# Kernel optimization log

Measured on AMD Instinct MI355X. Metric: run time of the kernel, lower is better.

## Reference

```python
import jax, jax.numpy as jnp
import numpy as np

B, N, H = 64, 512, 1024
NH = 8            # attention heads
HD = H // NH      # head dim
STEPS = 24


def setup_inputs() -> dict:
    key = jax.random.key(0)
    ks = jax.random.split(key, 12)
    s = 0.05  # weight scale to keep gates/softmax in a sane range
    return {
        "encoder_outputs": jax.random.normal(ks[0], (B, N, H), dtype=jnp.float32),
        "hidden": jax.random.normal(ks[1], (B, H), dtype=jnp.float32) * s,
        "cell": jax.random.normal(ks[2], (B, H), dtype=jnp.float32) * s,
        "end_node_embed": jax.random.normal(ks[3], (B, H), dtype=jnp.float32),
        "initial_input": jax.random.normal(ks[4], (B, 3 * H), dtype=jnp.float32),
        "max_steps": STEPS,
        # LSTMCell params (torch layout: [4H, in], gate order i,f,g,o)
        "W_ih": jax.random.normal(ks[5], (4 * H, 3 * H), dtype=jnp.float32) * s,
        "b_ih": jnp.zeros((4 * H,), jnp.float32),
        "W_hh": jax.random.normal(ks[6], (4 * H, H), dtype=jnp.float32) * s,
        "b_hh": jnp.zeros((4 * H,), jnp.float32),
        # MultiheadAttention params (torch in_proj [3H,H] = [Wq;Wk;Wv])
        "attn_in_w": jax.random.normal(ks[7], (3 * H, H), dtype=jnp.float32) * s,
        "attn_in_b": jnp.zeros((3 * H,), jnp.float32),
        "attn_out_w": jax.random.normal(ks[8], (H, H), dtype=jnp.float32) * s,
        "attn_out_b": jnp.zeros((H,), jnp.float32),
        # query_transform Linear
        "qt_w": jax.random.normal(ks[9], (H, H), dtype=jnp.float32) * s,
        "qt_b": jnp.zeros((H,), jnp.float32),
    }


def reference(encoder_outputs, hidden, cell, end_node_embed, initial_input,
              max_steps, W_ih, b_ih, W_hh, b_hh,
              attn_in_w, attn_in_b, attn_out_w, attn_out_b, qt_w, qt_b):
    b, n, h = encoder_outputs.shape
    nh, hd = NH, H // NH
    Wq, Wk, Wv = jnp.split(attn_in_w, 3, axis=0)
    bq, bk, bv = jnp.split(attn_in_b, 3)
    S = max_steps
    dt = encoder_outputs.dtype
    buf0 = jnp.zeros((b, S, h), dt)  # preallocated KV cache of decoder hiddens
    neg = jnp.asarray(-1e30, dt)
    scale = 1.0 / jnp.sqrt(jnp.asarray(hd, dt))
    pos = jnp.arange(S)

    def step(carry, t):
        hn, cn, x, buf = carry
        # --- LSTMCell (torch gate order i,f,g,o) ---
        gates = x @ W_ih.T + b_ih + hn @ W_hh.T + b_hh
        i, f, g, o = jnp.split(gates, 4, axis=-1)
        cn = jax.nn.sigmoid(f) * cn + jax.nn.sigmoid(i) * jnp.tanh(g)
        hn = jax.nn.sigmoid(o) * jnp.tanh(cn)
        buf = buf.at[:, t, :].set(hn)
        # --- causal self-attention: q = current hidden, kv = all hiddens <= t ---
        q = (hn @ Wq.T + bq).reshape(b, nh, hd)
        k = (buf @ Wk.T + bk).reshape(b, S, nh, hd)
        v = (buf @ Wv.T + bv).reshape(b, S, nh, hd)
        scores = jnp.einsum('bhd,bshd->bhs', q, k) * scale
        scores = jnp.where((pos > t)[None, None, :], neg, scores)
        attn = jax.nn.softmax(scores, axis=-1)
        ctx = jnp.einsum('bhs,bshd->bhd', attn, v).reshape(b, h)
        attn_out = ctx @ attn_out_w.T + attn_out_b
        # --- pointer scoring ---
        query = (0.5 * (hn + attn_out)) @ qt_w.T + qt_b
        logits = jnp.einsum('bh,bnh->bn', query, encoder_outputs)  # [B,N]
        _, idx = jax.lax.top_k(logits, 3)
        idx = jnp.sort(idx, axis=1)
        top3 = jnp.take_along_axis(encoder_outputs, idx[:, :, None], axis=1)  # [B,3,H]
        x = top3.reshape(b, 3 * h)
        return (hn, cn, x, buf), (logits, idx)

    _, (logits, idx) = jax.lax.scan(
        step, (hidden, cell, initial_input, buf0), jnp.arange(S))
    return logits, idx  # [max_steps,B,N], [max_steps,B,3]
```

## Files before the change

kernel.cpp:

```cpp
#include <hip/hip_runtime.h>
#include <math.h>

#define B_  64
#define N_  512
#define H_  1024
#define NH_ 8
#define HD_ 128
#define S_  24

__global__ __launch_bounds__(256) void wc_pre(
    const float* __restrict__ Wqt, const float* __restrict__ Wout,
    const float* __restrict__ bout, const float* __restrict__ bqt,
    float* __restrict__ W2, float* __restrict__ bc)
{
  __shared__ float As[16][68];
  __shared__ float Bs[16][68];
  const int tid = threadIdx.x;
  const int k0 = (blockIdx.x & 15) * 64;
  const int n0 = (blockIdx.x >> 4) * 64;
  const int tn = tid & 15, tm = tid >> 4;

#pragma unroll
  for (int i = 0; i < 4; ++i) {
    int n = n0 + tm * 4 + i;
    float4 w = *(const float4*)(Wqt + (size_t)n * 1024 + k0 + tn * 4);
    *(float4*)(W2 + (size_t)n * 2048 + k0 + tn * 4) =
        make_float4(0.5f * w.x, 0.5f * w.y, 0.5f * w.z, 0.5f * w.w);
  }

  float acc[4][4];
#pragma unroll
  for (int i = 0; i < 4; ++i)
#pragma unroll
    for (int j = 0; j < 4; ++j) acc[i][j] = 0.f;

  for (int m0 = 0; m0 < 1024; m0 += 16) {
    {
      int nn = tid >> 2, mm = (tid & 3) * 4;
      float4 a = *(const float4*)(Wqt + (size_t)(n0 + nn) * 1024 + m0 + mm);
      As[mm + 0][nn] = a.x; As[mm + 1][nn] = a.y;
      As[mm + 2][nn] = a.z; As[mm + 3][nn] = a.w;
      int mr = tid >> 4, kc = (tid & 15) * 4;
      float4 b = *(const float4*)(Wout + (size_t)(m0 + mr) * 1024 + k0 + kc);
      *(float4*)(&Bs[mr][kc]) = b;
    }
    __syncthreads();
#pragma unroll
    for (int m = 0; m < 16; ++m) {
      float av[4], bv[4];
      *(float4*)av = *(const float4*)(&As[m][tm * 4]);
      *(float4*)bv = *(const float4*)(&Bs[m][tn * 4]);
#pragma unroll
      for (int i = 0; i < 4; ++i)
#pragma unroll
        for (int j = 0; j < 4; ++j)
          acc[i][j] = fmaf(av[i], bv[j], acc[i][j]);
    }
    __syncthreads();
  }
#pragma unroll
  for (int i = 0; i < 4; ++i) {
    int n = n0 + tm * 4 + i;
    *(float4*)(W2 + (size_t)n * 2048 + 1024 + k0 + tn * 4) =
        make_float4(0.5f * acc[i][0], 0.5f * acc[i][1],
                    0.5f * acc[i][2], 0.5f * acc[i][3]);
  }

  {
    int w = tid >> 6, lane = tid & 63;
    int n = blockIdx.x * 4 + w;
    const float* row = Wqt + (size_t)n * 1024;
    float s = 0.f;
#pragma unroll
    for (int c = 0; c < 4; ++c) {
      float4 a = *(const float4*)(row + lane * 16 + c * 4);
      float4 b = *(const float4*)(bout + lane * 16 + c * 4);
      s = fmaf(a.x, b.x, fmaf(a.y, b.y, fmaf(a.z, b.z, fmaf(a.w, b.w, s))));
    }
#pragma unroll
    for (int off = 32; off > 0; off >>= 1) s += __shfl_down(s, off, 64);
    if (lane == 0) bc[n] = 0.5f * s + bqt[n];
  }
}

__device__ __forceinline__ float sigm(float x) { return 1.f / (1.f + expf(-x)); }

__device__ __forceinline__ void ins3(float v, int i,
    float& v0, int& i0, float& v1, int& i1, float& v2, int& i2)
{
  if (v > v0 || (v == v0 && i < i0)) {
    v2 = v1; i2 = i1; v1 = v0; i1 = i0; v0 = v; i0 = i;
  } else if (v > v1 || (v == v1 && i < i1)) {
    v2 = v1; i2 = i1; v1 = v; i1 = i;
  } else if (v > v2 || (v == v2 && i < i2)) {
    v2 = v; i2 = i;
  }
}

__global__ __launch_bounds__(512, 2) void gemm5(
    const float* __restrict__ A0, int ldA0, const float* __restrict__ W0, int ldW0,
    int K0,
    const float* __restrict__ A1, int ldA1, const float* __restrict__ W1, int ldW1,
    const float* __restrict__ enc, const int* __restrict__ idxi, int gather,
    float* __restrict__ P, int N, int KS)
{
  __shared__ float As[16 * 68];
  __shared__ float Bs[16 * 132];
  const int tid = threadIdx.x;
  const int nb = blockIdx.x, sp = blockIdx.y;
  const int ks = sp * KS;

  const float* A; const float* W; int ldA, ldW, koff; int seg0;
  if (ks < K0) { A = A0; W = W0; ldA = ldA0; ldW = ldW0; koff = ks; seg0 = 1; }
  else { A = A1; W = W1; ldA = ldA1; ldW = ldW1; koff = ks - K0; seg0 = 0; }

  const int tn = tid & 31, tm = tid >> 5;
  const int lr = tid >> 2, lc = (tid & 3) * 4;

  float acc[4][4];
#pragma unroll
  for (int i = 0; i < 4; ++i)
#pragma unroll
    for (int j = 0; j < 4; ++j) acc[i][j] = 0.f;

  const float* Wrow = W + (size_t)(nb * 128 + lr) * ldW + koff + lc;
  const float* Arow = nullptr;
  if (tid < 256) {
    if (seg0 && gather) {
      int ei = idxi[lr * 3 + (koff >> 10)];
      Arow = enc + ((size_t)lr * 512 + ei) * 1024 + (koff & 1023) + lc;
    } else {
      Arow = A + (size_t)lr * ldA + koff + lc;
    }
  }

  for (int k0 = 0; k0 < KS; k0 += 16) {
    float4 b4 = *(const float4*)(Wrow + k0);
    if (tid < 256) {
      float4 a4 = *(const float4*)(Arow + k0);
      As[(lc + 0) * 68 + lr] = a4.x; As[(lc + 1) * 68 + lr] = a4.y;
      As[(lc + 2) * 68 + lr] = a4.z; As[(lc + 3) * 68 + lr] = a4.w;
    }
    Bs[(lc + 0) * 132 + lr] = b4.x; Bs[(lc + 1) * 132 + lr] = b4.y;
    Bs[(lc + 2) * 132 + lr] = b4.z; Bs[(lc + 3) * 132 + lr] = b4.w;
    __syncthreads();
#pragma unroll
    for (int k = 0; k < 16; ++k) {
      float av[4], bv[4];
      *(float4*)av = *(const float4*)(As + k * 68 + tm * 4);
      *(float4*)bv = *(const float4*)(Bs + k * 132 + tn * 4);
#pragma unroll
      for (int i = 0; i < 4; ++i)
#pragma unroll
        for (int j = 0; j < 4; ++j)
          acc[i][j] = fmaf(av[i], bv[j], acc[i][j]);
    }
    __syncthreads();
  }
  float* Pb = P + (size_t)sp * 64 * N + nb * 128;
#pragma unroll
  for (int i = 0; i < 4; ++i)
    *(float4*)(Pb + (size_t)(tm * 4 + i) * N + tn * 4) =
        make_float4(acc[i][0], acc[i][1], acc[i][2], acc[i][3]);
}

__global__ __launch_bounds__(256) void lstm_red(
    const float* __restrict__ P, const float* __restrict__ b_ih,
    const float* __restrict__ b_hh, const float* __restrict__ c_in,
    float* __restrict__ h_out, float* __restrict__ c_out)
{
  int idx = blockIdx.x * 256 + threadIdx.x;
  int b = idx >> 8, j4 = (idx & 255) * 4;
  float g[4][4];
#pragma unroll
  for (int c = 0; c < 4; ++c) {
    int n = c * 1024 + j4;
    float4 s = *(const float4*)(b_ih + n);
    float4 s2 = *(const float4*)(b_hh + n);
    s.x += s2.x; s.y += s2.y; s.z += s2.z; s.w += s2.w;
#pragma unroll
    for (int sp = 0; sp < 8; ++sp) {
      float4 v = *(const float4*)(P + ((size_t)sp * 64 + b) * 4096 + n);
      s.x += v.x; s.y += v.y; s.z += v.z; s.w += v.w;
    }
    g[c][0] = s.x; g[c][1] = s.y; g[c][2] = s.z; g[c][3] = s.w;
  }
  float4 cp = *(const float4*)(c_in + b * 1024 + j4);
  float cv[4] = {cp.x, cp.y, cp.z, cp.w};
  float4 ho, co;
  float* hp = &ho.x; float* cpn = &co.x;
#pragma unroll
  for (int e = 0; e < 4; ++e) {
    float c = sigm(g[1][e]) * cv[e] + sigm(g[0][e]) * tanhf(g[2][e]);
    cpn[e] = c;
    hp[e] = sigm(g[3][e]) * tanhf(c);
  }
  *(float4*)(c_out + b * 1024 + j4) = co;
  *(float4*)(h_out + b * 1024 + j4) = ho;
}

__global__ __launch_bounds__(128) void attn_fused(
    const float* __restrict__ P, const float* __restrict__ bqkv,
    float* __restrict__ Kc, float* __restrict__ Vc,
    float* __restrict__ ctx, int t)
{
  const float scale = 0.08838834764831845f;
  int bh = blockIdx.x;
  int b = bh >> 3, h = bh & 7;
  int d = threadIdx.x;
  __shared__ float qs[128];
  __shared__ float sc[S_];

  const float* Pb = P + (size_t)b * 3072 + h * 128 + d;
  float qv = bqkv[h * 128 + d];
  float kv = bqkv[1024 + h * 128 + d];
  float vv = bqkv[2048 + h * 128 + d];
#pragma unroll
  for (int sp = 0; sp < 8; ++sp) {
    const float* pp = Pb + (size_t)sp * 64 * 3072;
    qv += pp[0]; kv += pp[1024]; vv += pp[2048];
  }
  float* Kb = Kc + (size_t)(b * NH_ + h) * S_ * HD_;
  float* Vb = Vc + (size_t)(b * NH_ + h) * S_ * HD_;
  Kb[t * 128 + d] = kv;
  Vb[t * 128 + d] = vv;
  qs[d] = qv;
  __syncthreads();

  int wave = d >> 6, lane = d & 63;
  for (int s = wave; s <= t; s += 2) {
    float pr = qs[lane] * Kb[s * 128 + lane] + qs[lane + 64] * Kb[s * 128 + lane + 64];
#pragma unroll
    for (int off = 32; off > 0; off >>= 1) pr += __shfl_down(pr, off, 64);
    if (lane == 0) sc[s] = pr * scale;
  }
  __syncthreads();

  float m = -3.4e38f;
  for (int s = 0; s <= t; ++s) m = fmaxf(m, sc[s]);
  float den = 0.f;
  for (int s = 0; s <= t; ++s) den += expf(sc[s] - m);
  float acc = 0.f;
  for (int s = 0; s <= t; ++s) acc += expf(sc[s] - m) * Vb[s * 128 + d];
  ctx[(size_t)b * 1024 + h * 128 + d] = acc / den;
}

__global__ __launch_bounds__(256) void logits4(
    const float* __restrict__ P, const float* __restrict__ bc,
    const float* __restrict__ enc, float* __restrict__ out,
    float* __restrict__ candv, int* __restrict__ candi)
{
  __shared__ float qs[1024];
  __shared__ float cv[12];
  __shared__ int   ci[12];
  const int tid = threadIdx.x;
  const int b = blockIdx.x >> 4, ng = blockIdx.x & 15;

  {
    const int j4 = tid * 4;
    float4 s = *(const float4*)(bc + j4);
#pragma unroll
    for (int sp = 0; sp < 16; ++sp) {
      float4 v = *(const float4*)(P + ((size_t)sp * 64 + b) * 1024 + j4);
      s.x += v.x; s.y += v.y; s.z += v.z; s.w += v.w;
    }
    *(float4*)(qs + j4) = s;
  }
  __syncthreads();

  const int wave = tid >> 6, lane = tid & 63;
  float4 q0 = *(const float4*)(qs + lane * 4);
  float4 q1 = *(const float4*)(qs + 256 + lane * 4);
  float4 q2 = *(const float4*)(qs + 512 + lane * 4);
  float4 q3 = *(const float4*)(qs + 768 + lane * 4);

  const int row0 = ng * 32 + wave * 8;
  const float* eb = enc + ((size_t)b * N_ + row0) * 1024 + lane * 4;
  float* lo = out + (size_t)b * N_ + row0;
  float v0 = -3.4e38f, v1 = -3.4e38f, v2 = -3.4e38f;
  int i0 = 0x7fffffff, i1 = 0x7fffffff, i2 = 0x7fffffff;
  float myout = 0.f;
#pragma unroll
  for (int r = 0; r < 8; r += 2) {
    const float* ea = eb + (size_t)r * 1024;
    const float* eb2 = eb + (size_t)(r + 1) * 1024;
    float4 a0 = *(const float4*)(ea);
    float4 a1 = *(const float4*)(ea + 256);
    float4 a2 = *(const float4*)(ea + 512);
    float4 a3 = *(const float4*)(ea + 768);
    float4 b0 = *(const float4*)(eb2);
    float4 b1 = *(const float4*)(eb2 + 256);
    float4 b2 = *(const float4*)(eb2 + 512);
    float4 b3 = *(const float4*)(eb2 + 768);
    float s0 = 0.f, s1 = 0.f;
    s0 = fmaf(q0.x, a0.x, s0); s1 = fmaf(q0.x, b0.x, s1);
    s0 = fmaf(q0.y, a0.y, s0); s1 = fmaf(q0.y, b0.y, s1);
    s0 = fmaf(q0.z, a0.z, s0); s1 = fmaf(q0.z, b0.z, s1);
    s0 = fmaf(q0.w, a0.w, s0); s1 = fmaf(q0.w, b0.w, s1);
    s0 = fmaf(q1.x, a1.x, s0); s1 = fmaf(q1.x, b1.x, s1);
    s0 = fmaf(q1.y, a1.y, s0); s1 = fmaf(q1.y, b1.y, s1);
    s0 = fmaf(q1.z, a1.z, s0); s1 = fmaf(q1.z, b1.z, s1);
    s0 = fmaf(q1.w, a1.w, s0); s1 = fmaf(q1.w, b1.w, s1);
    s0 = fmaf(q2.x, a2.x, s0); s1 = fmaf(q2.x, b2.x, s1);
    s0 = fmaf(q2.y, a2.y, s0); s1 = fmaf(q2.y, b2.y, s1);
    s0 = fmaf(q2.z, a2.z, s0); s1 = fmaf(q2.z, b2.z, s1);
    s0 = fmaf(q2.w, a2.w, s0); s1 = fmaf(q2.w, b2.w, s1);
    s0 = fmaf(q3.x, a3.x, s0); s1 = fmaf(q3.x, b3.x, s1);
    s0 = fmaf(q3.y, a3.y, s0); s1 = fmaf(q3.y, b3.y, s1);
    s0 = fmaf(q3.z, a3.z, s0); s1 = fmaf(q3.z, b3.z, s1);
    s0 = fmaf(q3.w, a3.w, s0); s1 = fmaf(q3.w, b3.w, s1);
#pragma unroll
    for (int off = 32; off > 0; off >>= 1) {
      s0 += __shfl_xor(s0, off, 64);
      s1 += __shfl_xor(s1, off, 64);
    }
    if (lane == r) myout = s0;
    if (lane == r + 1) myout = s1;
    ins3(s0, row0 + r, v0, i0, v1, i1, v2, i2);
    ins3(s1, row0 + r + 1, v0, i0, v1, i1, v2, i2);
  }
  if (lane < 8) lo[lane] = myout;
  if (lane == 0) {
    cv[wave * 3 + 0] = v0; ci[wave * 3 + 0] = i0;
    cv[wave * 3 + 1] = v1; ci[wave * 3 + 1] = i1;
    cv[wave * 3 + 2] = v2; ci[wave * 3 + 2] = i2;
  }
  __syncthreads();
  if (tid == 0) {
    float w0 = -3.4e38f, w1 = -3.4e38f, w2 = -3.4e38f;
    int j0 = 0x7fffffff, j1 = 0x7fffffff, j2 = 0x7fffffff;
#pragma unroll
    for (int k = 0; k < 12; ++k)
      ins3(cv[k], ci[k], w0, j0, w1, j1, w2, j2);
    candv[blockIdx.x * 3 + 0] = w0; candi[blockIdx.x * 3 + 0] = j0;
    candv[blockIdx.x * 3 + 1] = w1; candi[blockIdx.x * 3 + 1] = j1;
    candv[blockIdx.x * 3 + 2] = w2; candi[blockIdx.x * 3 + 2] = j2;
  }
}

__global__ __launch_bounds__(64) void top3_merge(
    const float* __restrict__ candv, const int* __restrict__ candi,
    float* __restrict__ idx_out, int* __restrict__ idxi)
{
  int b = threadIdx.x;
  float v0 = -3.4e38f, v1 = -3.4e38f, v2 = -3.4e38f;
  int i0 = 0x7fffffff, i1 = 0x7fffffff, i2 = 0x7fffffff;
  const int base = b * 48;
#pragma unroll
  for (int k = 0; k < 48; ++k)
    ins3(candv[base + k], candi[base + k], v0, i0, v1, i1, v2, i2);
  int a = i0, bb = i1, c = i2, tw;
  if (a > bb) { tw = a; a = bb; bb = tw; }
  if (bb > c) { tw = bb; bb = c; c = tw; }
  if (a > bb) { tw = a; a = bb; bb = tw; }
  idxi[b * 3 + 0] = a; idxi[b * 3 + 1] = bb; idxi[b * 3 + 2] = c;
  idx_out[b * 3 + 0] = (float)a;
  idx_out[b * 3 + 1] = (float)bb;
  idx_out[b * 3 + 2] = (float)c;
}

extern "C" void kernel_launch(void* const* d_in, const int* in_sizes, int n_in,
                              void* d_out, int out_size, void* d_ws, size_t ws_size,
                              hipStream_t stream)
{
  (void)in_sizes; (void)n_in; (void)out_size; (void)ws_size;
  const float* enc   = (const float*)d_in[0];
  const float* h0    = (const float*)d_in[1];
  const float* c0    = (const float*)d_in[2];
  const float* x0    = (const float*)d_in[4];
  const float* W_ih  = (const float*)d_in[6];
  const float* b_ih  = (const float*)d_in[7];
  const float* W_hh  = (const float*)d_in[8];
  const float* b_hh  = (const float*)d_in[9];
  const float* Wqkv  = (const float*)d_in[10];
  const float* bqkv  = (const float*)d_in[11];
  const float* Wout  = (const float*)d_in[12];
  const float* bout  = (const float*)d_in[13];
  const float* Wqt   = (const float*)d_in[14];
  const float* bqt   = (const float*)d_in[15];

  float* ws    = (float*)d_ws;
  float* P     = ws;
  float* W2    = P + 8 * 64 * 4096;
  float* bc    = W2 + 1024 * 2048;
  float* hbuf  = bc + 1024;
  float* cbuf  = hbuf + 64 * 1024;
  float* ctx   = cbuf + 64 * 1024;
  float* Kc    = ctx + 64 * 1024;
  float* Vc    = Kc + 64 * NH_ * S_ * HD_;
  float* candv = Vc + 64 * NH_ * S_ * HD_;
  int*   candi = (int*)(candv + 1024 * 3);
  int*   idxi  = candi + 1024 * 3;

  float* logits_out = (float*)d_out;
  float* idx_out    = logits_out + (size_t)S_ * B_ * N_;

  wc_pre<<<dim3(256), dim3(256), 0, stream>>>(Wqt, Wout, bout, bqt, W2, bc);

  for (int t = 0; t < S_; ++t) {
    const float* xin   = (t == 0) ? x0 : nullptr;
    const float* hprev = (t == 0) ? h0 : hbuf;
    const float* cprev = (t == 0) ? c0 : cbuf;

    gemm5<<<dim3(32, 8), dim3(512), 0, stream>>>(
        xin, 3072, W_ih, 3072, 3072,
        hprev, 1024, W_hh, 1024,
        enc, idxi, t > 0, P, 4096, 512);
    lstm_red<<<dim3(64), dim3(256), 0, stream>>>(P, b_ih, b_hh, cprev, hbuf, cbuf);

    gemm5<<<dim3(24, 8), dim3(512), 0, stream>>>(
        hbuf, 1024, Wqkv, 1024, 1024,
        hbuf, 1024, Wqkv, 1024,
        enc, idxi, 0, P, 3072, 128);
    attn_fused<<<dim3(512), dim3(128), 0, stream>>>(P, bqkv, Kc, Vc, ctx, t);

    gemm5<<<dim3(8, 16), dim3(512), 0, stream>>>(
        hbuf, 1024, W2, 2048, 1024,
        ctx, 1024, W2 + 1024, 2048,
        enc, idxi, 0, P, 1024, 128);

    logits4<<<dim3(1024), dim3(256), 0, stream>>>(
        P, bc, enc, logits_out + (size_t)t * B_ * N_, candv, candi);
    top3_merge<<<dim3(1), dim3(64), 0, stream>>>(
        candv, candi, idx_out + (size_t)t * B_ * 3, idxi);
  }
}
```

Measured before the change: 3.802 ms.

## Double split-K in GEMMs and add register prefetch to GEMM and logits

Every split-K GEMM now uses twice as many K splits, each covering half the previous slice. This gives more blocks to fill the GPU, and the reduction loops in lstm_red, attn_fused and logits4 are widened to sum the extra partials. The GEMM inner loop now loads the next K-tile of A and W into registers while computing the current tile. The logits kernel prefetches the next pair of encoder rows the same way, which uses more registers and more partial-sum traffic in exchange for latency hiding.

```diff
diff --git a/kernel.cpp b/kernel.cpp
--- a/kernel.cpp
+++ b/kernel.cpp
@@ -134,16 +134,22 @@
     }
   }
 
+  float4 b4 = *(const float4*)(Wrow);
+  float4 a4 = make_float4(0.f, 0.f, 0.f, 0.f);
+  if (tid < 256) a4 = *(const float4*)(Arow);
+
   for (int k0 = 0; k0 < KS; k0 += 16) {
-    float4 b4 = *(const float4*)(Wrow + k0);
     if (tid < 256) {
-      float4 a4 = *(const float4*)(Arow + k0);
       As[(lc + 0) * 68 + lr] = a4.x; As[(lc + 1) * 68 + lr] = a4.y;
       As[(lc + 2) * 68 + lr] = a4.z; As[(lc + 3) * 68 + lr] = a4.w;
     }
     Bs[(lc + 0) * 132 + lr] = b4.x; Bs[(lc + 1) * 132 + lr] = b4.y;
     Bs[(lc + 2) * 132 + lr] = b4.z; Bs[(lc + 3) * 132 + lr] = b4.w;
     __syncthreads();
+    if (k0 + 16 < KS) {
+      b4 = *(const float4*)(Wrow + k0 + 16);
+      if (tid < 256) a4 = *(const float4*)(Arow + k0 + 16);
+    }
 #pragma unroll
     for (int k = 0; k < 16; ++k) {
       float av[4], bv[4];
@@ -179,7 +185,7 @@
     float4 s2 = *(const float4*)(b_hh + n);
     s.x += s2.x; s.y += s2.y; s.z += s2.z; s.w += s2.w;
 #pragma unroll
-    for (int sp = 0; sp < 8; ++sp) {
+    for (int sp = 0; sp < 16; ++sp) {
       float4 v = *(const float4*)(P + ((size_t)sp * 64 + b) * 4096 + n);
       s.x += v.x; s.y += v.y; s.z += v.z; s.w += v.w;
     }
@@ -216,7 +222,7 @@
   float kv = bqkv[1024 + h * 128 + d];
   float vv = bqkv[2048 + h * 128 + d];
 #pragma unroll
-  for (int sp = 0; sp < 8; ++sp) {
+  for (int sp = 0; sp < 16; ++sp) {
     const float* pp = Pb + (size_t)sp * 64 * 3072;
     qv += pp[0]; kv += pp[1024]; vv += pp[2048];
   }
@@ -245,6 +251,22 @@
   ctx[(size_t)b * 1024 + h * 128 + d] = acc / den;
 }
 
+__device__ __forceinline__ float dot16(
+    const float4& q0, const float4& q1, const float4& q2, const float4& q3,
+    const float4& e0, const float4& e1, const float4& e2, const float4& e3)
+{
+  float s = 0.f;
+  s = fmaf(q0.x, e0.x, s); s = fmaf(q0.y, e0.y, s);
+  s = fmaf(q0.z, e0.z, s); s = fmaf(q0.w, e0.w, s);
+  s = fmaf(q1.x, e1.x, s); s = fmaf(q1.y, e1.y, s);
+  s = fmaf(q1.z, e1.z, s); s = fmaf(q1.w, e1.w, s);
+  s = fmaf(q2.x, e2.x, s); s = fmaf(q2.y, e2.y, s);
+  s = fmaf(q2.z, e2.z, s); s = fmaf(q2.w, e2.w, s);
+  s = fmaf(q3.x, e3.x, s); s = fmaf(q3.y, e3.y, s);
+  s = fmaf(q3.z, e3.z, s); s = fmaf(q3.w, e3.w, s);
+  return s;
+}
+
 __global__ __launch_bounds__(256) void logits4(
     const float* __restrict__ P, const float* __restrict__ bc,
     const float* __restrict__ enc, float* __restrict__ out,
@@ -260,7 +282,7 @@
     const int j4 = tid * 4;
     float4 s = *(const float4*)(bc + j4);
 #pragma unroll
-    for (int sp = 0; sp < 16; ++sp) {
+    for (int sp = 0; sp < 32; ++sp) {
       float4 v = *(const float4*)(P + ((size_t)sp * 64 + b) * 1024 + j4);
       s.x += v.x; s.y += v.y; s.z += v.z; s.w += v.w;
     }
@@ -280,35 +302,33 @@
   float v0 = -3.4e38f, v1 = -3.4e38f, v2 = -3.4e38f;
   int i0 = 0x7fffffff, i1 = 0x7fffffff, i2 = 0x7fffffff;
   float myout = 0.f;
-#pragma unroll
-  for (int r = 0; r < 8; r += 2) {
-    const float* ea = eb + (size_t)r * 1024;
-    const float* eb2 = eb + (size_t)(r + 1) * 1024;
-    float4 a0 = *(const float4*)(ea);
-    float4 a1 = *(const float4*)(ea + 256);
-    float4 a2 = *(const float4*)(ea + 512);
-    float4 a3 = *(const float4*)(ea + 768);
-    float4 b0 = *(const float4*)(eb2);
-    float4 b1 = *(const float4*)(eb2 + 256);
-    float4 b2 = *(const float4*)(eb2 + 512);
-    float4 b3 = *(const float4*)(eb2 + 768);
-    float s0 = 0.f, s1 = 0.f;
-    s0 = fmaf(q0.x, a0.x, s0); s1 = fmaf(q0.x, b0.x, s1);
-    s0 = fmaf(q0.y, a0.y, s0); s1 = fmaf(q0.y, b0.y, s1);
-    s0 = fmaf(q0.z, a0.z, s0); s1 = fmaf(q0.z, b0.z, s1);
-    s0 = fmaf(q0.w, a0.w, s0); s1 = fmaf(q0.w, b0.w, s1);
-    s0 = fmaf(q1.x, a1.x, s0); s1 = fmaf(q1.x, b1.x, s1);
-    s0 = fmaf(q1.y, a1.y, s0); s1 = fmaf(q1.y, b1.y, s1);
-    s0 = fmaf(q1.z, a1.z, s0); s1 = fmaf(q1.z, b1.z, s1);
-    s0 = fmaf(q1.w, a1.w, s0); s1 = fmaf(q1.w, b1.w, s1);
-    s0 = fmaf(q2.x, a2.x, s0); s1 = fmaf(q2.x, b2.x, s1);
-    s0 = fmaf(q2.y, a2.y, s0); s1 = fmaf(q2.y, b2.y, s1);
-    s0 = fmaf(q2.z, a2.z, s0); s1 = fmaf(q2.z, b2.z, s1);
-    s0 = fmaf(q2.w, a2.w, s0); s1 = fmaf(q2.w, b2.w, s1);
-    s0 = fmaf(q3.x, a3.x, s0); s1 = fmaf(q3.x, b3.x, s1);
-    s0 = fmaf(q3.y, a3.y, s0); s1 = fmaf(q3.y, b3.y, s1);
-    s0 = fmaf(q3.z, a3.z, s0); s1 = fmaf(q3.z, b3.z, s1);
-    s0 = fmaf(q3.w, a3.w, s0); s1 = fmaf(q3.w, b3.w, s1);
+
+  float4 A0 = *(const float4*)(eb);
+  float4 A1 = *(const float4*)(eb + 256);
+  float4 A2 = *(const float4*)(eb + 512);
+  float4 A3 = *(const float4*)(eb + 768);
+  float4 A4 = *(const float4*)(eb + 1024);
+  float4 A5 = *(const float4*)(eb + 1280);
+  float4 A6 = *(const float4*)(eb + 1536);
+  float4 A7 = *(const float4*)(eb + 1792);
+
+#pragma unroll
+  for (int p = 0; p < 4; ++p) {
+    const int r = p * 2;
+    float4 B0, B1, B2, B3, B4, B5, B6, B7;
+    if (p < 3) {
+      const float* ea = eb + (size_t)(r + 2) * 1024;
+      B0 = *(const float4*)(ea);
+      B1 = *(const float4*)(ea + 256);
+      B2 = *(const float4*)(ea + 512);
+      B3 = *(const float4*)(ea + 768);
+      B4 = *(const float4*)(ea + 1024);
+      B5 = *(const float4*)(ea + 1280);
+      B6 = *(const float4*)(ea + 1536);
+      B7 = *(const float4*)(ea + 1792);
+    }
+    float s0 = dot16(q0, q1, q2, q3, A0, A1, A2, A3);
+    float s1 = dot16(q0, q1, q2, q3, A4, A5, A6, A7);
 #pragma unroll
     for (int off = 32; off > 0; off >>= 1) {
       s0 += __shfl_xor(s0, off, 64);
@@ -318,6 +338,10 @@
     if (lane == r + 1) myout = s1;
     ins3(s0, row0 + r, v0, i0, v1, i1, v2, i2);
     ins3(s1, row0 + r + 1, v0, i0, v1, i1, v2, i2);
+    if (p < 3) {
+      A0 = B0; A1 = B1; A2 = B2; A3 = B3;
+      A4 = B4; A5 = B5; A6 = B6; A7 = B7;
+    }
   }
   if (lane < 8) lo[lane] = myout;
   if (lane == 0) {
@@ -381,7 +405,7 @@
 
   float* ws    = (float*)d_ws;
   float* P     = ws;
-  float* W2    = P + 8 * 64 * 4096;
+  float* W2    = P + 16 * 64 * 4096;
   float* bc    = W2 + 1024 * 2048;
   float* hbuf  = bc + 1024;
   float* cbuf  = hbuf + 64 * 1024;
@@ -402,22 +426,22 @@
     const float* hprev = (t == 0) ? h0 : hbuf;
     const float* cprev = (t == 0) ? c0 : cbuf;
 
-    gemm5<<<dim3(32, 8), dim3(512), 0, stream>>>(
+    gemm5<<<dim3(32, 16), dim3(512), 0, stream>>>(
         xin, 3072, W_ih, 3072, 3072,
         hprev, 1024, W_hh, 1024,
-        enc, idxi, t > 0, P, 4096, 512);
+        enc, idxi, t > 0, P, 4096, 256);
     lstm_red<<<dim3(64), dim3(256), 0, stream>>>(P, b_ih, b_hh, cprev, hbuf, cbuf);
 
-    gemm5<<<dim3(24, 8), dim3(512), 0, stream>>>(
+    gemm5<<<dim3(24, 16), dim3(512), 0, stream>>>(
         hbuf, 1024, Wqkv, 1024, 1024,
         hbuf, 1024, Wqkv, 1024,
-        enc, idxi, 0, P, 3072, 128);
+        enc, idxi, 0, P, 3072, 64);
     attn_fused<<<dim3(512), dim3(128), 0, stream>>>(P, bqkv, Kc, Vc, ctx, t);
 
-    gemm5<<<dim3(8, 16), dim3(512), 0, stream>>>(
+    gemm5<<<dim3(8, 32), dim3(512), 0, stream>>>(
         hbuf, 1024, W2, 2048, 1024,
         ctx, 1024, W2 + 1024, 2048,
-        enc, idxi, 0, P, 1024, 128);
+        enc, idxi, 0, P, 1024, 64);
 
     logits4<<<dim3(1024), dim3(256), 0, stream>>>(
         P, bc, enc, logits_out + (size_t)t * B_ * N_, candv, candi);
```

Measured after the change: 3.811 ms. No clear change (+0.2%).
